# Kernel optimization log

Measured on AMD Instinct MI355X. Metric: run time of the kernel, lower is better.

Reference implementation:

```python
import jax, jax.numpy as jnp
import numpy as np

N = 50000      # nodes
E = 800000     # edges (before self loops)
F_IN = 128     # dataset.num_features
HID = 32       # hidden_channels (per GAT head)
HEADS = 4
C = 40         # dataset.num_classes
NEG_SLOPE = 0.2


def setup_inputs() -> dict:
    key = jax.random.key(0)
    ks = jax.random.split(key, 18)
    g = lambda k, shape, fan: jax.random.normal(k, shape, dtype=jnp.float32) / np.sqrt(fan)
    inp = {
        "x": jax.random.normal(ks[0], (N, F_IN), dtype=jnp.float32),
        "edge_index": jax.random.randint(ks[1], (2, E), 0, N, dtype=jnp.int64),
        # GAT layer 1: F_IN -> HEADS*HID
        "gat_W1": g(ks[2], (F_IN, HEADS * HID), F_IN),
        "gat_att_src1": g(ks[3], (HEADS, HID), HID),
        "gat_att_dst1": g(ks[4], (HEADS, HID), HID),
        "gat_b1": jnp.zeros((HEADS * HID,), jnp.float32),
        # GAT layer 2: HEADS*HID -> C, heads=1
        "gat_W2": g(ks[5], (HEADS * HID, C), HEADS * HID),
        "gat_att_src2": g(ks[6], (1, C), C),
        "gat_att_dst2": g(ks[7], (1, C), C),
        "gat_b2": jnp.zeros((C,), jnp.float32),
        # GCN layers
        "gcn_W1": g(ks[8], (F_IN, HID), F_IN),
        "gcn_b1": jnp.zeros((HID,), jnp.float32),
        "gcn_W2": g(ks[9], (HID, C), HID),
        "gcn_b2": jnp.zeros((C,), jnp.float32),
        # final linear: 2C -> C
        "lin_W": g(ks[10], (2 * C, C), 2 * C),
        "lin_b": jnp.zeros((C,), jnp.float32),
        "weight_c": jnp.float32(0.5),
        "weight_t": jnp.float32(0.5),
    }
    return inp


def _add_self_loops(src, dst, n):
    loop = jnp.arange(n, dtype=src.dtype)
    return jnp.concatenate([src, loop]), jnp.concatenate([dst, loop])


def _gat_conv(x, src, dst, n, W, att_src, att_dst, b, heads, out_dim):
    # h: [n, heads, out_dim]
    h = (x @ W).reshape(n, heads, out_dim)
    a_s = jnp.einsum('nhd,hd->nh', h, att_src)   # source-side attention logit
    a_d = jnp.einsum('nhd,hd->nh', h, att_dst)   # target-side attention logit
    e = jax.nn.leaky_relu(a_s[src] + a_d[dst], NEG_SLOPE)  # [E', heads]
    # softmax over incoming edges of each target node (self loops guarantee >=1 edge)
    m = jax.ops.segment_max(e, dst, num_segments=n)
    ex = jnp.exp(e - m[dst])
    s = jax.ops.segment_sum(ex, dst, num_segments=n)
    alpha = ex / s[dst]                          # [E', heads]
    out = jax.ops.segment_sum(h[src] * alpha[..., None], dst, num_segments=n)
    return out.reshape(n, heads * out_dim) + b


def _gcn_conv(x, src, dst, n, W, b):
    h = x @ W
    deg = jax.ops.segment_sum(jnp.ones(src.shape, h.dtype), dst, num_segments=n)
    norm = jax.lax.rsqrt(deg)                    # deg >= 1 (self loops)
    coef = (norm[src] * norm[dst])[:, None]
    return jax.ops.segment_sum(h[src] * coef, dst, num_segments=n) + b


def reference(x, edge_index, gat_W1, gat_att_src1, gat_att_dst1, gat_b1,
              gat_W2, gat_att_src2, gat_att_dst2, gat_b2,
              gcn_W1, gcn_b1, gcn_W2, gcn_b2, lin_W, lin_b,
              weight_c, weight_t):
    n = x.shape[0]
    src, dst = _add_self_loops(edge_index[0], edge_index[1], n)
    # GAT branch (dropout is identity at inference)
    x_gat = _gat_conv(x, src, dst, n, gat_W1, gat_att_src1, gat_att_dst1,
                      gat_b1, HEADS, HID)
    x_gat = jax.nn.elu(x_gat)
    x_gat = _gat_conv(x_gat, src, dst, n, gat_W2, gat_att_src2, gat_att_dst2,
                      gat_b2, 1, C)
    # GCN branch
    x_gcn = jax.nn.relu(_gcn_conv(x, src, dst, n, gcn_W1, gcn_b1))
    x_gcn = _gcn_conv(x_gcn, src, dst, n, gcn_W2, gcn_b2)
    # weighted feature concat + linear head
    cat = jnp.concatenate([x_gcn * weight_c, x_gat * weight_t], axis=1)  # [n, 2C]
    return cat @ lin_W + lin_b
```

## Files before the change

### kernel.cpp

```cpp
#include <hip/hip_runtime.h>
#include <math.h>

#define F_IN   128
#define HIDC   32
#define NHEAD  4
#define CDIM   40
#define NEG_SLOPE 0.2f
#define BCAP   4096
#define OVCAP  16384
#define SCHUNK 4096

__device__ __forceinline__ float leakyf(float x) { return x > 0.f ? x : NEG_SLOPE * x; }

__device__ __forceinline__ float wred_max(float v) {
#pragma unroll
    for (int o = 32; o > 0; o >>= 1) v = fmaxf(v, __shfl_xor(v, o, 64));
    return v;
}
__device__ __forceinline__ float wred_sum(float v) {
#pragma unroll
    for (int o = 32; o > 0; o >>= 1) v += __shfl_xor(v, o, 64);
    return v;
}
__device__ __forceinline__ float sel4(float4 v, int h) {
    return (h == 0) ? v.x : (h == 1) ? v.y : (h == 2) ? v.z : v.w;
}
__device__ __forceinline__ unsigned pack2_bf16(float a, float b) {
    unsigned ua = __float_as_uint(a);
    unsigned ub = __float_as_uint(b);
    ua = (ua + 0x7FFFu + ((ua >> 16) & 1u)) >> 16;
    ub = (ub + 0x7FFFu + ((ub >> 16) & 1u)) >> 16;
    return ua | (ub << 16);
}
__device__ __forceinline__ float2 unpack2_bf16(unsigned p) {
    return make_float2(__uint_as_float(p << 16), __uint_as_float(p & 0xFFFF0000u));
}

__global__ __launch_bounds__(640) void gemm1_fused_kernel(
    const float* __restrict__ X, const float* __restrict__ Wg,
    const float* __restrict__ Wc, unsigned* __restrict__ h1b,
    unsigned* __restrict__ g1b, int n)
{
    constexpr int BN = 64, BK = 32, CG = 40, NT = 640;
    __shared__ float Xs[BK][BN + 4];
    __shared__ float Ws[BK][160];
    const int tid = threadIdx.x;
    const int cg = tid % CG, ng = tid / CG;
    const int node0 = blockIdx.x * BN;
    float acc[4][4] = {};

    for (int kb = 0; kb < 128; kb += BK) {
        for (int idx = tid; idx < BN * (BK / 4); idx += NT) {
            int nd = idx / (BK / 4);
            int kq = idx % (BK / 4);
            int gnode = node0 + nd;
            float4 v = (gnode < n) ? *(const float4*)&X[(size_t)gnode * 128 + kb + kq * 4]
                                   : make_float4(0.f, 0.f, 0.f, 0.f);
            Xs[kq * 4 + 0][nd] = v.x;
            Xs[kq * 4 + 1][nd] = v.y;
            Xs[kq * 4 + 2][nd] = v.z;
            Xs[kq * 4 + 3][nd] = v.w;
        }
        for (int idx = tid; idx < BK * CG; idx += NT) {
            int kk = idx / CG;
            int cq = idx % CG;
            float4 v = (cq < 32) ? *(const float4*)&Wg[(size_t)(kb + kk) * 128 + cq * 4]
                                 : *(const float4*)&Wc[(size_t)(kb + kk) * 32 + (cq - 32) * 4];
            *(float4*)&Ws[kk][cq * 4] = v;
        }
        __syncthreads();
#pragma unroll
        for (int k = 0; k < BK; ++k) {
            float4 xv = *(const float4*)&Xs[k][ng * 4];
            float4 wv = *(const float4*)&Ws[k][cg * 4];
            float xa[4] = {xv.x, xv.y, xv.z, xv.w};
            float wa[4] = {wv.x, wv.y, wv.z, wv.w};
#pragma unroll
            for (int j = 0; j < 4; ++j)
#pragma unroll
                for (int c = 0; c < 4; ++c)
                    acc[j][c] = fmaf(xa[j], wa[c], acc[j][c]);
        }
        __syncthreads();
    }
#pragma unroll
    for (int j = 0; j < 4; ++j) {
        int gnode = node0 + ng * 4 + j;
        if (gnode >= n) continue;
        uint2 pb = make_uint2(pack2_bf16(acc[j][0], acc[j][1]),
                              pack2_bf16(acc[j][2], acc[j][3]));
        if (cg < 32) *(uint2*)&h1b[(size_t)gnode * 64 + cg * 2] = pb;
        else         *(uint2*)&g1b[(size_t)gnode * 16 + (cg - 32) * 2] = pb;
    }
}

template<int K, int OUTC, int BN, int BK, int OSTRIDE = OUTC>
__global__ __launch_bounds__((OUTC / 4) * (BN / 4)) void gemm_tile(
    const float* __restrict__ X, const float* __restrict__ W,
    const float* __restrict__ bias, float* __restrict__ Y, int n)
{
    constexpr int CG = OUTC / 4;
    constexpr int NG = BN / 4;
    constexpr int NT = CG * NG;
    __shared__ float Xs[BK][BN + 4];
    __shared__ float Ws[BK][OUTC];
    const int tid = threadIdx.x;
    const int cg = tid % CG, ng = tid / CG;
    const int node0 = blockIdx.x * BN;
    float acc[4][4] = {};

    for (int kb = 0; kb < K; kb += BK) {
        for (int idx = tid; idx < BN * (BK / 4); idx += NT) {
            int nd = idx / (BK / 4);
            int kq = idx % (BK / 4);
            int gnode = node0 + nd;
            float4 v = (gnode < n) ? *(const float4*)&X[(size_t)gnode * K + kb + kq * 4]
                                   : make_float4(0.f, 0.f, 0.f, 0.f);
            Xs[kq * 4 + 0][nd] = v.x;
            Xs[kq * 4 + 1][nd] = v.y;
            Xs[kq * 4 + 2][nd] = v.z;
            Xs[kq * 4 + 3][nd] = v.w;
        }
        for (int idx = tid; idx < BK * CG; idx += NT) {
            int kk = idx / CG;
            int cq = idx % CG;
            *(float4*)&Ws[kk][cq * 4] = *(const float4*)&W[(size_t)(kb + kk) * OUTC + cq * 4];
        }
        __syncthreads();
#pragma unroll
        for (int k = 0; k < BK; ++k) {
            float4 xv = *(const float4*)&Xs[k][ng * 4];
            float4 wv = *(const float4*)&Ws[k][cg * 4];
            float xa[4] = {xv.x, xv.y, xv.z, xv.w};
            float wa[4] = {wv.x, wv.y, wv.z, wv.w};
#pragma unroll
            for (int j = 0; j < 4; ++j)
#pragma unroll
                for (int c = 0; c < 4; ++c)
                    acc[j][c] = fmaf(xa[j], wa[c], acc[j][c]);
        }
        __syncthreads();
    }

    float4 bv = make_float4(0.f, 0.f, 0.f, 0.f);
    if (bias) bv = *(const float4*)&bias[cg * 4];
#pragma unroll
    for (int j = 0; j < 4; ++j) {
        int gnode = node0 + ng * 4 + j;
        if (gnode < n) {
            float4 o = make_float4(acc[j][0] + bv.x, acc[j][1] + bv.y,
                                   acc[j][2] + bv.z, acc[j][3] + bv.w);
            *(float4*)&Y[(size_t)gnode * OSTRIDE + cg * 4] = o;
        }
    }
}

template<int K, int OUTC, int BN, int BK, int OSTRIDE_U, int OFF_U>
__global__ __launch_bounds__((OUTC / 4) * (BN / 4)) void gemm_tile_b(
    const float* __restrict__ X, const float* __restrict__ W,
    unsigned* __restrict__ Yb, int n)
{
    constexpr int CG = OUTC / 4;
    constexpr int NG = BN / 4;
    constexpr int NT = CG * NG;
    __shared__ float Xs[BK][BN + 4];
    __shared__ float Ws[BK][OUTC];
    const int tid = threadIdx.x;
    const int cg = tid % CG, ng = tid / CG;
    const int node0 = blockIdx.x * BN;
    float acc[4][4] = {};

    for (int kb = 0; kb < K; kb += BK) {
        for (int idx = tid; idx < BN * (BK / 4); idx += NT) {
            int nd = idx / (BK / 4);
            int kq = idx % (BK / 4);
            int gnode = node0 + nd;
            float4 v = (gnode < n) ? *(const float4*)&X[(size_t)gnode * K + kb + kq * 4]
                                   : make_float4(0.f, 0.f, 0.f, 0.f);
            Xs[kq * 4 + 0][nd] = v.x;
            Xs[kq * 4 + 1][nd] = v.y;
            Xs[kq * 4 + 2][nd] = v.z;
            Xs[kq * 4 + 3][nd] = v.w;
        }
        for (int idx = tid; idx < BK * CG; idx += NT) {
            int kk = idx / CG;
            int cq = idx % CG;
            *(float4*)&Ws[kk][cq * 4] = *(const float4*)&W[(size_t)(kb + kk) * OUTC + cq * 4];
        }
        __syncthreads();
#pragma unroll
        for (int k = 0; k < BK; ++k) {
            float4 xv = *(const float4*)&Xs[k][ng * 4];
            float4 wv = *(const float4*)&Ws[k][cg * 4];
            float xa[4] = {xv.x, xv.y, xv.z, xv.w};
            float wa[4] = {wv.x, wv.y, wv.z, wv.w};
#pragma unroll
            for (int j = 0; j < 4; ++j)
#pragma unroll
                for (int c = 0; c < 4; ++c)
                    acc[j][c] = fmaf(xa[j], wa[c], acc[j][c]);
        }
        __syncthreads();
    }

#pragma unroll
    for (int j = 0; j < 4; ++j) {
        int gnode = node0 + ng * 4 + j;
        if (gnode < n) {
            uint2 pb = make_uint2(pack2_bf16(acc[j][0], acc[j][1]),
                                  pack2_bf16(acc[j][2], acc[j][3]));
            *(uint2*)&Yb[(size_t)gnode * OSTRIDE_U + OFF_U + cg * 2] = pb;
        }
    }
}

template<int K, int OUTC, int BN, int BK, int OSTRIDE_U, int OFF_U>
__global__ __launch_bounds__((OUTC / 4) * (BN / 4)) void gemm_tile_bb(
    const unsigned* __restrict__ Xb, const float* __restrict__ W,
    unsigned* __restrict__ Yb, int n)
{
    constexpr int CG = OUTC / 4;
    constexpr int NG = BN / 4;
    constexpr int NT = CG * NG;
    __shared__ float Xs[BK][BN + 4];
    __shared__ float Ws[BK][OUTC];
    const int tid = threadIdx.x;
    const int cg = tid % CG, ng = tid / CG;
    const int node0 = blockIdx.x * BN;
    float acc[4][4] = {};

    for (int kb = 0; kb < K; kb += BK) {
        for (int idx = tid; idx < BN * (BK / 8); idx += NT) {
            int nd = idx / (BK / 8);
            int kq = idx % (BK / 8);
            int gnode = node0 + nd;
            uint4 v = (gnode < n) ? *(const uint4*)&Xb[(size_t)gnode * (K / 2) + kb / 2 + kq * 4]
                                  : make_uint4(0u, 0u, 0u, 0u);
            float2 a = unpack2_bf16(v.x), b = unpack2_bf16(v.y);
            float2 c = unpack2_bf16(v.z), d = unpack2_bf16(v.w);
            Xs[kq * 8 + 0][nd] = a.x; Xs[kq * 8 + 1][nd] = a.y;
            Xs[kq * 8 + 2][nd] = b.x; Xs[kq * 8 + 3][nd] = b.y;
            Xs[kq * 8 + 4][nd] = c.x; Xs[kq * 8 + 5][nd] = c.y;
            Xs[kq * 8 + 6][nd] = d.x; Xs[kq * 8 + 7][nd] = d.y;
        }
        for (int idx = tid; idx < BK * CG; idx += NT) {
            int kk = idx / CG;
            int cq = idx % CG;
            *(float4*)&Ws[kk][cq * 4] = *(const float4*)&W[(size_t)(kb + kk) * OUTC + cq * 4];
        }
        __syncthreads();
#pragma unroll
        for (int k = 0; k < BK; ++k) {
            float4 xv = *(const float4*)&Xs[k][ng * 4];
            float4 wv = *(const float4*)&Ws[k][cg * 4];
            float xa[4] = {xv.x, xv.y, xv.z, xv.w};
            float wa[4] = {wv.x, wv.y, wv.z, wv.w};
#pragma unroll
            for (int j = 0; j < 4; ++j)
#pragma unroll
                for (int c = 0; c < 4; ++c)
                    acc[j][c] = fmaf(xa[j], wa[c], acc[j][c]);
        }
        __syncthreads();
    }

#pragma unroll
    for (int j = 0; j < 4; ++j) {
        int gnode = node0 + ng * 4 + j;
        if (gnode < n) {
            uint2 pb = make_uint2(pack2_bf16(acc[j][0], acc[j][1]),
                                  pack2_bf16(acc[j][2], acc[j][3]));
            *(uint2*)&Yb[(size_t)gnode * OSTRIDE_U + OFF_U + cg * 2] = pb;
        }
    }
}

__global__ __launch_bounds__(256) void bucket_scatter_kernel(
    const int* __restrict__ src, const int* __restrict__ dst,
    unsigned* __restrict__ bcnt, unsigned* __restrict__ bpair,
    unsigned* __restrict__ ovf_cnt, uint2* __restrict__ ovf, int e, int nbuck)
{
    __shared__ unsigned hist[512];
    __shared__ unsigned base[512];
    const int t = threadIdx.x;
    const int lo = blockIdx.x * SCHUNK;
    const int hi = min(lo + SCHUNK, e);
    for (int i = t; i < nbuck; i += 256) hist[i] = 0;
    __syncthreads();
    for (int i = lo + t; i < hi; i += 256)
        atomicAdd(&hist[((unsigned)dst[i]) >> 7], 1u);
    __syncthreads();
    for (int i = t; i < nbuck; i += 256) {
        unsigned c = hist[i];
        base[i] = c ? atomicAdd(&bcnt[i], c) : 0u;
        hist[i] = 0;
    }
    __syncthreads();
    for (int i = lo + t; i < hi; i += 256) {
        unsigned s = (unsigned)src[i], d = (unsigned)dst[i];
        unsigned b = d >> 7;
        unsigned pos = base[b] + atomicAdd(&hist[b], 1u);
        if (pos < BCAP) bpair[(size_t)b * BCAP + pos] = s | ((d & 127u) << 16);
        else {
            unsigned o = atomicAdd(ovf_cnt, 1u);
            if (o < OVCAP) ovf[o] = make_uint2(s, d);
        }
    }
}

__global__ __launch_bounds__(256) void bucket_count_kernel(
    const unsigned* __restrict__ bcnt, const unsigned* __restrict__ bpair,
    const unsigned* __restrict__ ovf_cnt, const uint2* __restrict__ ovf,
    unsigned* __restrict__ counts, int n)
{
    __shared__ unsigned lc[128];
    const int b = blockIdx.x, base = b << 7;
    if (threadIdx.x < 128) lc[threadIdx.x] = 0;
    __syncthreads();
    unsigned bc = bcnt[b];
    int cnt = (int)(bc < BCAP ? bc : BCAP);
    for (int k = threadIdx.x; k < cnt; k += 256)
        atomicAdd(&lc[bpair[(size_t)b * BCAP + k] >> 16], 1u);
    unsigned oc_u = *ovf_cnt;
    int oc = (int)(oc_u < OVCAP ? oc_u : OVCAP);
    for (int k = threadIdx.x; k < oc; k += 256) {
        uint2 pp = ovf[k];
        if ((int)(pp.y >> 7) == b) atomicAdd(&lc[pp.y & 127u], 1u);
    }
    __syncthreads();
    int i = base + threadIdx.x;
    if (threadIdx.x < 128 && i < n) counts[i] = lc[threadIdx.x];
}

__global__ __launch_bounds__(256) void scan_reduce_kernel(const unsigned* __restrict__ counts,
                                                          unsigned* __restrict__ partials, int n)
{
    __shared__ unsigned sm[256];
    int t = threadIdx.x;
    int i = blockIdx.x * 256 + t;
    unsigned v = (i < n) ? counts[i] : 0u;
    sm[t] = v;
    __syncthreads();
#pragma unroll
    for (int off = 128; off > 0; off >>= 1) {
        if (t < off) sm[t] += sm[t + off];
        __syncthreads();
    }
    if (t == 0) partials[blockIdx.x] = sm[0];
}

__global__ __launch_bounds__(256) void scan_partials_kernel(unsigned* __restrict__ partials,
                                                            unsigned* __restrict__ rs, int nb, int n)
{
    __shared__ unsigned sm[256];
    int t = threadIdx.x;
    unsigned v = (t < nb) ? partials[t] : 0u;
    sm[t] = v;
    __syncthreads();
#pragma unroll
    for (int off = 1; off < 256; off <<= 1) {
        unsigned u = (t >= off) ? sm[t - off] : 0u;
        __syncthreads();
        sm[t] += u;
        __syncthreads();
    }
    if (t < nb) partials[t] = sm[t] - v;
    if (t == 255) rs[n] = sm[255];
}

__global__ __launch_bounds__(256) void scan_write_kernel(const unsigned* __restrict__ counts,
                                                         const unsigned* __restrict__ partials,
                                                         unsigned* __restrict__ rs,
                                                         float* __restrict__ nrm, int n)
{
    __shared__ unsigned sm[256];
    int t = threadIdx.x;
    int i = blockIdx.x * 256 + t;
    unsigned c = (i < n) ? counts[i] : 0u;
    sm[t] = c;
    __syncthreads();
#pragma unroll
    for (int off = 1; off < 256; off <<= 1) {
        unsigned u = (t >= off) ? sm[t - off] : 0u;
        __syncthreads();
        sm[t] += u;
        __syncthreads();
    }
    if (i < n) {
        rs[i] = partials[blockIdx.x] + sm[t] - c;
        nrm[i] = rsqrtf((float)(c + 1u));
    }
}

__global__ __launch_bounds__(256) void bucket_place_kernel(
    const unsigned* __restrict__ bcnt, const unsigned* __restrict__ bpair,
    const unsigned* __restrict__ rs, unsigned* __restrict__ csr_src,
    unsigned* __restrict__ cursor, int n)
{
    __shared__ unsigned lc[128];
    __shared__ unsigned rbase[128];
    const int b = blockIdx.x, base = b << 7;
    if (threadIdx.x < 128) {
        lc[threadIdx.x] = 0;
        int i = base + threadIdx.x;
        rbase[threadIdx.x] = (i < n) ? rs[i] : 0u;
    }
    __syncthreads();
    unsigned bc = bcnt[b];
    int cnt = (int)(bc < BCAP ? bc : BCAP);
    for (int k = threadIdx.x; k < cnt; k += 256) {
        unsigned v = bpair[(size_t)b * BCAP + k];
        unsigned ld = v >> 16;
        unsigned r = atomicAdd(&lc[ld], 1u);
        csr_src[rbase[ld] + r] = v & 0xFFFFu;
    }
    __syncthreads();
    int i = base + threadIdx.x;
    if (threadIdx.x < 128 && i < n) cursor[i] = rbase[threadIdx.x] + lc[threadIdx.x];
}

__global__ void overflow_fill_kernel(const unsigned* __restrict__ ovf_cnt,
                                     const uint2* __restrict__ ovf,
                                     unsigned* __restrict__ cursor,
                                     unsigned* __restrict__ csr_src)
{
    unsigned oc_u = *ovf_cnt;
    int oc = (int)(oc_u < OVCAP ? oc_u : OVCAP);
    for (int k = threadIdx.x; k < oc; k += 256) {
        uint2 pp = ovf[k];
        unsigned pos = atomicAdd(&cursor[pp.y], 1u);
        csr_src[pos] = pp.x;
    }
}

__global__ void logits1_kernel(const unsigned* __restrict__ h1b, const float* __restrict__ aw_s,
                               const float* __restrict__ aw_d, float* __restrict__ as1,
                               float* __restrict__ ad1, int n)
{
    __shared__ float sw[128], dw[128];
    if (threadIdx.x < 128) { sw[threadIdx.x] = aw_s[threadIdx.x]; dw[threadIdx.x] = aw_d[threadIdx.x]; }
    __syncthreads();
    int idx = blockIdx.x * 256 + threadIdx.x;
    if (idx >= n * NHEAD) return;
    int node = idx >> 2, h = idx & 3;
    const unsigned* row = h1b + (size_t)node * 64 + h * 16;
    float s = 0.f, d = 0.f;
#pragma unroll
    for (int k = 0; k < 16; ++k) {
        float2 v = unpack2_bf16(row[k]);
        int c = h * HIDC + 2 * k;
        s = fmaf(v.x, sw[c], s);     s = fmaf(v.y, sw[c + 1], s);
        d = fmaf(v.x, dw[c], d);     d = fmaf(v.y, dw[c + 1], d);
    }
    as1[idx] = s; ad1[idx] = d;
}

__global__ void logits2_kernel(const unsigned* __restrict__ hg_b, const float* __restrict__ aw_s,
                               const float* __restrict__ aw_d, float* __restrict__ as2,
                               float* __restrict__ ad2, int n)
{
    __shared__ float sw[CDIM], dw[CDIM];
    if (threadIdx.x < CDIM) { sw[threadIdx.x] = aw_s[threadIdx.x]; dw[threadIdx.x] = aw_d[threadIdx.x]; }
    __syncthreads();
    int i = blockIdx.x * 256 + threadIdx.x;
    if (i >= n) return;
    const unsigned* row = hg_b + (size_t)i * 40;
    float s = 0.f, d = 0.f;
#pragma unroll
    for (int k = 0; k < 20; ++k) {
        float2 v = unpack2_bf16(row[k]);
        s = fmaf(v.x, sw[2 * k], s);     s = fmaf(v.y, sw[2 * k + 1], s);
        d = fmaf(v.x, dw[2 * k], d);     d = fmaf(v.y, dw[2 * k + 1], d);
    }
    as2[i] = s; ad2[i] = d;
}

#define CAP1 96
__global__ __launch_bounds__(256) void gat_agg1_kernel(
    const unsigned* __restrict__ h1b,
    const float* __restrict__ as1, const float* __restrict__ ad1,
    const unsigned* __restrict__ rs, const unsigned* __restrict__ csr_src,
    const float* __restrict__ b1, unsigned* __restrict__ xgb, int n)
{
    __shared__ unsigned sidx[4][CAP1];
    __shared__ float    w4[4][CAP1][4];
    const int wid = threadIdx.x >> 6;
    const int lane = threadIdx.x & 63;
    const int i = blockIdx.x * 4 + wid;
    if (i >= n) return;
    const unsigned beg = rs[i];
    const int deg = (int)(rs[i + 1] - beg);
    const float4* as1v = (const float4*)as1;
    float4 av = as1v[i];
    float4 dv = ((const float4*)ad1)[i];
    float4 es = make_float4(leakyf(av.x + dv.x), leakyf(av.y + dv.y),
                            leakyf(av.z + dv.z), leakyf(av.w + dv.w));
    float m0 = es.x, m1 = es.y, m2 = es.z, m3 = es.w;
    for (int k = lane; k < deg; k += 64) {
        unsigned s = csr_src[beg + k];
        float4 a = as1v[s];
        float e0 = leakyf(a.x + dv.x), e1 = leakyf(a.y + dv.y);
        float e2 = leakyf(a.z + dv.z), e3 = leakyf(a.w + dv.w);
        if (k < CAP1) {
            sidx[wid][k] = s;
            w4[wid][k][0] = e0; w4[wid][k][1] = e1;
            w4[wid][k][2] = e2; w4[wid][k][3] = e3;
        }
        m0 = fmaxf(m0, e0); m1 = fmaxf(m1, e1);
        m2 = fmaxf(m2, e2); m3 = fmaxf(m3, e3);
    }
    m0 = wred_max(m0); m1 = wred_max(m1); m2 = wred_max(m2); m3 = wred_max(m3);
    float s0 = 0.f, s1 = 0.f, s2 = 0.f, s3 = 0.f;
    if (lane == 0) {
        s0 = __expf(es.x - m0); s1 = __expf(es.y - m1);
        s2 = __expf(es.z - m2); s3 = __expf(es.w - m3);
    }
    const int dc = deg < CAP1 ? deg : CAP1;
    for (int k = lane; k < dc; k += 64) {
        float w0 = __expf(w4[wid][k][0] - m0); w4[wid][k][0] = w0; s0 += w0;
        float w1 = __expf(w4[wid][k][1] - m1); w4[wid][k][1] = w1; s1 += w1;
        float w2 = __expf(w4[wid][k][2] - m2); w4[wid][k][2] = w2; s2 += w2;
        float w3 = __expf(w4[wid][k][3] - m3); w4[wid][k][3] = w3; s3 += w3;
    }
    for (int k = CAP1 + lane; k < deg; k += 64) {
        unsigned s = csr_src[beg + k];
        float4 a = as1v[s];
        s0 += __expf(leakyf(a.x + dv.x) - m0);
        s1 += __expf(leakyf(a.y + dv.y) - m1);
        s2 += __expf(leakyf(a.z + dv.z) - m2);
        s3 += __expf(leakyf(a.w + dv.w) - m3);
    }
    s0 = wred_sum(s0); s1 = wred_sum(s1); s2 = wred_sum(s2); s3 = wred_sum(s3);
    __threadfence_block();
    const int h = lane >> 4;
    const float mh   = sel4(make_float4(m0, m1, m2, m3), h);
    const float advh = sel4(dv, h);
    const float ssh  = sel4(make_float4(s0, s1, s2, s3), h);
    const float wself = __expf(sel4(es, h) - mh);
    float2 hv = unpack2_bf16(h1b[(size_t)i * 64 + lane]);
    float2 acc = make_float2(hv.x * wself, hv.y * wself);
    auto edge = [&](int j, unsigned& s, float& w) {
        if (j < CAP1) { s = sidx[wid][j]; w = w4[wid][j][h]; }
        else {
            s = csr_src[beg + j];
            float4 a = as1v[s];
            w = __expf(leakyf(sel4(a, h) + advh) - mh);
        }
    };
    int j = 0;
    for (; j + 4 <= deg; j += 4) {
        unsigned sa, sb, sc, sd; float wa, wb, wc, wd;
        edge(j, sa, wa); edge(j + 1, sb, wb); edge(j + 2, sc, wc); edge(j + 3, sd, wd);
        float2 va = unpack2_bf16(h1b[(size_t)sa * 64 + lane]);
        float2 vb = unpack2_bf16(h1b[(size_t)sb * 64 + lane]);
        float2 vc = unpack2_bf16(h1b[(size_t)sc * 64 + lane]);
        float2 vd = unpack2_bf16(h1b[(size_t)sd * 64 + lane]);
        acc.x = fmaf(va.x, wa, acc.x); acc.y = fmaf(va.y, wa, acc.y);
        acc.x = fmaf(vb.x, wb, acc.x); acc.y = fmaf(vb.y, wb, acc.y);
        acc.x = fmaf(vc.x, wc, acc.x); acc.y = fmaf(vc.y, wc, acc.y);
        acc.x = fmaf(vd.x, wd, acc.x); acc.y = fmaf(vd.y, wd, acc.y);
    }
    for (; j < deg; ++j) {
        unsigned s; float w; edge(j, s, w);
        float2 v = unpack2_bf16(h1b[(size_t)s * 64 + lane]);
        acc.x = fmaf(v.x, w, acc.x); acc.y = fmaf(v.y, w, acc.y);
    }
    float inv = 1.f / ssh;
    int c0 = 2 * lane;
    float o0 = acc.x * inv + b1[c0];
    float o1 = acc.y * inv + b1[c0 + 1];
    o0 = o0 > 0.f ? o0 : __expf(o0) - 1.f;
    o1 = o1 > 0.f ? o1 : __expf(o1) - 1.f;
    xgb[(size_t)i * 64 + lane] = pack2_bf16(o0, o1);
}

#define CAP2 128
__global__ __launch_bounds__(256) void agg2_fused_kernel(
    const unsigned* __restrict__ hg_b, const float* __restrict__ as2,
    const float* __restrict__ ad2, const float* __restrict__ nrm,
    const unsigned* __restrict__ rs, const unsigned* __restrict__ csr_src,
    const float* __restrict__ gat_b2, const float* __restrict__ gcn_b2,
    const float* __restrict__ wc_p, const float* __restrict__ wt_p,
    float* __restrict__ cat, int n)
{
    __shared__ unsigned sidx[4][CAP2];
    __shared__ float    wgt[4][CAP2];
    __shared__ float    cf [4][CAP2];
    const int wid = threadIdx.x >> 6;
    const int lane = threadIdx.x & 63;
    const int i = blockIdx.x * 4 + wid;
    if (i >= n) return;
    const unsigned beg = rs[i];
    const int deg = (int)(rs[i + 1] - beg);
    const float adv = ad2[i];
    const float e_self = leakyf(as2[i] + adv);
    const float ni = nrm[i];
    float m = e_self;
    for (int k = lane; k < deg; k += 64) {
        unsigned s = csr_src[beg + k];
        float e = leakyf(as2[s] + adv);
        if (k < CAP2) { sidx[wid][k] = s; wgt[wid][k] = e; cf[wid][k] = nrm[s]; }
        m = fmaxf(m, e);
    }
    m = wred_max(m);
    float ssum = (lane == 0) ? __expf(e_self - m) : 0.f;
    const int dc = deg < CAP2 ? deg : CAP2;
    for (int k = lane; k < dc; k += 64) {
        float w = __expf(wgt[wid][k] - m);
        wgt[wid][k] = w; ssum += w;
    }
    for (int k = CAP2 + lane; k < deg; k += 64) {
        unsigned s = csr_src[beg + k];
        ssum += __expf(leakyf(as2[s] + adv) - m);
    }
    ssum = wred_sum(ssum);
    __threadfence_block();
    const bool act   = lane < 40;
    const bool isgat = lane < 20;
    const float selfw = isgat ? __expf(e_self - m) : ni * ni;
    float2 acc = make_float2(0.f, 0.f);
    if (act) {
        float2 v = unpack2_bf16(hg_b[(size_t)i * 40 + lane]);
        acc.x = v.x * selfw; acc.y = v.y * selfw;
    }
    auto edge = [&](int j, unsigned& s, float& w) {
        if (j < CAP2) {
            s = sidx[wid][j];
            w = isgat ? wgt[wid][j] : cf[wid][j] * ni;
        } else {
            s = csr_src[beg + j];
            w = isgat ? __expf(leakyf(as2[s] + adv) - m) : nrm[s] * ni;
        }
    };
    int j = 0;
    for (; j + 4 <= deg; j += 4) {
        unsigned sa, sb, sc, sd; float wa, wb, wc, wd;
        edge(j, sa, wa); edge(j + 1, sb, wb); edge(j + 2, sc, wc); edge(j + 3, sd, wd);
        if (act) {
            float2 va = unpack2_bf16(hg_b[(size_t)sa * 40 + lane]);
            float2 vb = unpack2_bf16(hg_b[(size_t)sb * 40 + lane]);
            float2 vc = unpack2_bf16(hg_b[(size_t)sc * 40 + lane]);
            float2 vd = unpack2_bf16(hg_b[(size_t)sd * 40 + lane]);
            acc.x = fmaf(va.x, wa, acc.x); acc.y = fmaf(va.y, wa, acc.y);
            acc.x = fmaf(vb.x, wb, acc.x); acc.y = fmaf(vb.y, wb, acc.y);
            acc.x = fmaf(vc.x, wc, acc.x); acc.y = fmaf(vc.y, wc, acc.y);
            acc.x = fmaf(vd.x, wd, acc.x); acc.y = fmaf(vd.y, wd, acc.y);
        }
    }
    for (; j < deg; ++j) {
        unsigned s; float w; edge(j, s, w);
        if (act) {
            float2 v = unpack2_bf16(hg_b[(size_t)s * 40 + lane]);
            acc.x = fmaf(v.x, w, acc.x); acc.y = fmaf(v.y, w, acc.y);
        }
    }
    if (act) {
        if (isgat) {
            float inv = 1.f / ssum, wt = *wt_p;
            int c0 = 2 * lane;
            cat[(size_t)i * 80 + 40 + c0]     = (acc.x * inv + gat_b2[c0]) * wt;
            cat[(size_t)i * 80 + 40 + c0 + 1] = (acc.y * inv + gat_b2[c0 + 1]) * wt;
        } else {
            float wc = *wc_p;
            int c0 = 2 * (lane - 20);
            cat[(size_t)i * 80 + c0]     = (acc.x + gcn_b2[c0]) * wc;
            cat[(size_t)i * 80 + c0 + 1] = (acc.y + gcn_b2[c0 + 1]) * wc;
        }
    }
}

#define CAPG 128
__global__ __launch_bounds__(256) void gcn_agg1_kernel(
    const unsigned short* __restrict__ g1b, const float* __restrict__ nrm,
    const unsigned* __restrict__ rs, const unsigned* __restrict__ csr_src,
    const float* __restrict__ b, float* __restrict__ out, int n)
{
    __shared__ unsigned sidx[4][CAPG];
    __shared__ float    cf[4][CAPG];
    const int wid = threadIdx.x >> 6;
    const int lane = threadIdx.x & 63;
    const int i = blockIdx.x * 4 + wid;
    if (i >= n) return;
    const unsigned beg = rs[i];
    const int deg = (int)(rs[i + 1] - beg);
    const float ni = nrm[i];
    const int dcg = deg < CAPG ? deg : CAPG;
    for (int k = lane; k < dcg; k += 64) {
        unsigned s = csr_src[beg + k];
        sidx[wid][k] = s; cf[wid][k] = nrm[s];
    }
    __threadfence_block();
    const int half = lane >> 5, c = lane & 31;
    auto ldb = [&](unsigned node) {
        return __uint_as_float(((unsigned)g1b[(size_t)node * 32 + c]) << 16);
    };
    float acc = (half == 0) ? ldb(i) * ni * ni : 0.f;
    auto edge = [&](int j, unsigned& s, float& w) {
        if (j < CAPG) { s = sidx[wid][j]; w = cf[wid][j] * ni; }
        else { s = csr_src[beg + j]; w = nrm[s] * ni; }
    };
    int j = half;
    for (; j + 2 < deg; j += 4) {
        unsigned sa, sb; float wa, wb;
        edge(j, sa, wa); edge(j + 2, sb, wb);
        float va = ldb(sa);
        float vb = ldb(sb);
        acc = fmaf(va, wa, acc);
        acc = fmaf(vb, wb, acc);
    }
    for (; j < deg; j += 2) {
        unsigned s; float w; edge(j, s, w);
        acc = fmaf(ldb(s), w, acc);
    }
    acc += __shfl_xor(acc, 32, 64);
    if (half == 0) out[(size_t)i * 32 + c] = fmaxf(acc + b[c], 0.f);
}

extern "C" void kernel_launch(void* const* d_in, const int* in_sizes, int n_in,
                              void* d_out, int out_size, void* d_ws, size_t ws_size,
                              hipStream_t stream)
{
    const float* x        = (const float*)d_in[0];
    const int*   eidx     = (const int*)d_in[1];
    const float* gat_W1   = (const float*)d_in[2];
    const float* att_s1   = (const float*)d_in[3];
    const float* att_d1   = (const float*)d_in[4];
    const float* gat_b1   = (const float*)d_in[5];
    const float* gat_W2   = (const float*)d_in[6];
    const float* att_s2   = (const float*)d_in[7];
    const float* att_d2   = (const float*)d_in[8];
    const float* gat_b2   = (const float*)d_in[9];
    const float* gcn_W1   = (const float*)d_in[10];
    const float* gcn_b1   = (const float*)d_in[11];
    const float* gcn_W2   = (const float*)d_in[12];
    const float* gcn_b2   = (const float*)d_in[13];
    const float* lin_W    = (const float*)d_in[14];
    const float* lin_b    = (const float*)d_in[15];
    const float* wc_p     = (const float*)d_in[16];
    const float* wt_p     = (const float*)d_in[17];

    const int n = in_sizes[0] / F_IN;
    const int e = in_sizes[1] / 2;
    const int* src = eidx;
    const int* dst = eidx + e;
    const int NBUCK = (n + 127) >> 7;

    char* p = (char*)d_ws;
    auto alloc = [&](size_t bytes) -> void* {
        void* r = (void*)p;
        p += (bytes + 255) & ~(size_t)255;
        return r;
    };
    unsigned* counts  = (unsigned*)alloc((size_t)n * 4);
    unsigned* rs      = (unsigned*)alloc((size_t)(n + 1) * 4);
    unsigned* cursor  = (unsigned*)alloc((size_t)n * 4);
    unsigned* partials= (unsigned*)alloc(256 * 4);
    unsigned* bcnt    = (unsigned*)alloc((size_t)(NBUCK + 1) * 4);
    unsigned* csr_src = (unsigned*)alloc((size_t)e * 4);
    float* nrm     = (float*)alloc((size_t)n * 4);
    float* as1     = (float*)alloc((size_t)n * 4 * 4);
    float* ad1     = (float*)alloc((size_t)n * 4 * 4);
    float* as2     = (float*)alloc((size_t)n * 4);
    float* ad2     = (float*)alloc((size_t)n * 4);
    float* cat     = (float*)alloc((size_t)n * 80 * 4);
    unsigned* hg_b = (unsigned*)alloc((size_t)n * 40 * 4);
    float* xg      = (float*)alloc((size_t)n * F_IN * 4);
    unsigned* g1b  = (unsigned*)alloc((size_t)n * 16 * 4);
    unsigned* bpair = (unsigned*)cat;
    uint2*    ovf   = (uint2*)(bpair + (size_t)NBUCK * BCAP);
    unsigned* h1b   = (unsigned*)cat;
    float*    gacc1 = xg;
    unsigned* xgb   = (unsigned*)xg;
    unsigned* ovf_cnt = bcnt + NBUCK;

    const int NB = (n + 255) / 256;
    const int WB = (n + 3) / 4;
    const int SB = (e + SCHUNK - 1) / SCHUNK;

    hipMemsetAsync(bcnt, 0, (size_t)(NBUCK + 1) * 4, stream);
    bucket_scatter_kernel<<<SB, 256, 0, stream>>>(src, dst, bcnt, bpair, ovf_cnt, ovf, e, NBUCK);
    bucket_count_kernel<<<NBUCK, 256, 0, stream>>>(bcnt, bpair, ovf_cnt, ovf, counts, n);
    scan_reduce_kernel<<<NB, 256, 0, stream>>>(counts, partials, n);
    scan_partials_kernel<<<1, 256, 0, stream>>>(partials, rs, NB, n);
    scan_write_kernel<<<NB, 256, 0, stream>>>(counts, partials, rs, nrm, n);
    bucket_place_kernel<<<NBUCK, 256, 0, stream>>>(bcnt, bpair, rs, csr_src, cursor, n);
    overflow_fill_kernel<<<1, 256, 0, stream>>>(ovf_cnt, ovf, cursor, csr_src);

    gemm1_fused_kernel<<<(n + 63) / 64, 640, 0, stream>>>(x, gat_W1, gcn_W1, h1b, g1b, n);

    gcn_agg1_kernel<<<WB, 256, 0, stream>>>((const unsigned short*)g1b, nrm, rs, csr_src,
                                            gcn_b1, gacc1, n);
    gemm_tile_b<32, 40, 128, 32, 40, 20><<<(n + 127) / 128, 320, 0, stream>>>(gacc1, gcn_W2, hg_b, n);

    logits1_kernel<<<(n * 4 + 255) / 256, 256, 0, stream>>>(h1b, att_s1, att_d1, as1, ad1, n);
    gat_agg1_kernel<<<WB, 256, 0, stream>>>(h1b, as1, ad1, rs, csr_src, gat_b1, xgb, n);
    gemm_tile_bb<128, 40, 128, 32, 40, 0><<<(n + 127) / 128, 320, 0, stream>>>(xgb, gat_W2, hg_b, n);
    logits2_kernel<<<NB, 256, 0, stream>>>(hg_b, att_s2, att_d2, as2, ad2, n);

    agg2_fused_kernel<<<WB, 256, 0, stream>>>(hg_b, as2, ad2, nrm, rs, csr_src,
                                              gat_b2, gcn_b2, wc_p, wt_p, cat, n);

    gemm_tile<80, 40, 128, 40><<<(n + 127) / 128, 320, 0, stream>>>(cat, lin_W, lin_b, (float*)d_out, n);
}
```

Baseline: 360.1 us.

## Use bf16 MFMA for first fused GEMM and fold layer-1 attention logits into it

Replaces the FP32 FMA tiled GEMM that computes the fused GAT/GCN first-layer projection with a bf16 MFMA (16x16x32) kernel, adding a small prep kernel that packs the weights into the MFMA B-fragment layout. The accumulated tile is staged in shared memory, and the per-head source/destination attention logits are computed there, which removes the separate logits1 kernel and its re-read of h1b. X is now rounded to bf16 before multiplication, so precision drops slightly compared to the FP32 accumulate path. An extra tiny kernel launch is added for the weight packing.

```diff
diff --git a/kernel.cpp b/kernel.cpp
--- a/kernel.cpp
+++ b/kernel.cpp
@@ -10,6 +10,9 @@
 #define OVCAP  16384
 #define SCHUNK 4096
 
+typedef __attribute__((ext_vector_type(8))) short bf16x8;
+typedef __attribute__((ext_vector_type(4))) float f32x4;
+
 __device__ __forceinline__ float leakyf(float x) { return x > 0.f ? x : NEG_SLOPE * x; }
 
 __device__ __forceinline__ float wred_max(float v) {
@@ -36,61 +39,96 @@
     return make_float2(__uint_as_float(p << 16), __uint_as_float(p & 0xFFFF0000u));
 }
 
-__global__ __launch_bounds__(640) void gemm1_fused_kernel(
-    const float* __restrict__ X, const float* __restrict__ Wg,
-    const float* __restrict__ Wc, unsigned* __restrict__ h1b,
-    unsigned* __restrict__ g1b, int n)
-{
-    constexpr int BN = 64, BK = 32, CG = 40, NT = 640;
-    __shared__ float Xs[BK][BN + 4];
-    __shared__ float Ws[BK][160];
+__global__ void wb_prep_kernel(const float* __restrict__ Wg, const float* __restrict__ Wc,
+                               uint4* __restrict__ wbf)
+{
+    int b = blockIdx.x;
+    int lane = threadIdx.x;
+    int nt = b >> 2, ks = b & 3;
+    int c = nt * 16 + (lane & 15);
+    int k0 = ks * 32 + (lane >> 4) * 8;
+    unsigned u[4];
+#pragma unroll
+    for (int jj = 0; jj < 4; ++jj) {
+        int k = k0 + 2 * jj;
+        float a0 = (c < 128) ? Wg[(size_t)k * 128 + c] : Wc[(size_t)k * 32 + (c - 128)];
+        float a1 = (c < 128) ? Wg[(size_t)(k + 1) * 128 + c] : Wc[(size_t)(k + 1) * 32 + (c - 128)];
+        u[jj] = pack2_bf16(a0, a1);
+    }
+    wbf[(size_t)b * 64 + lane] = make_uint4(u[0], u[1], u[2], u[3]);
+}
+
+__global__ __launch_bounds__(256) void gemm1_mfma_kernel(
+    const float* __restrict__ X, const uint4* __restrict__ wbf,
+    const float* __restrict__ aw_s, const float* __restrict__ aw_d,
+    unsigned* __restrict__ h1b, unsigned* __restrict__ g1b,
+    float* __restrict__ as1, float* __restrict__ ad1, int n)
+{
+    __shared__ float Ct[64][164];
+    __shared__ float sw[128], dw[128];
     const int tid = threadIdx.x;
-    const int cg = tid % CG, ng = tid / CG;
-    const int node0 = blockIdx.x * BN;
-    float acc[4][4] = {};
-
-    for (int kb = 0; kb < 128; kb += BK) {
-        for (int idx = tid; idx < BN * (BK / 4); idx += NT) {
-            int nd = idx / (BK / 4);
-            int kq = idx % (BK / 4);
-            int gnode = node0 + nd;
-            float4 v = (gnode < n) ? *(const float4*)&X[(size_t)gnode * 128 + kb + kq * 4]
-                                   : make_float4(0.f, 0.f, 0.f, 0.f);
-            Xs[kq * 4 + 0][nd] = v.x;
-            Xs[kq * 4 + 1][nd] = v.y;
-            Xs[kq * 4 + 2][nd] = v.z;
-            Xs[kq * 4 + 3][nd] = v.w;
-        }
-        for (int idx = tid; idx < BK * CG; idx += NT) {
-            int kk = idx / CG;
-            int cq = idx % CG;
-            float4 v = (cq < 32) ? *(const float4*)&Wg[(size_t)(kb + kk) * 128 + cq * 4]
-                                 : *(const float4*)&Wc[(size_t)(kb + kk) * 32 + (cq - 32) * 4];
-            *(float4*)&Ws[kk][cq * 4] = v;
-        }
-        __syncthreads();
-#pragma unroll
-        for (int k = 0; k < BK; ++k) {
-            float4 xv = *(const float4*)&Xs[k][ng * 4];
-            float4 wv = *(const float4*)&Ws[k][cg * 4];
-            float xa[4] = {xv.x, xv.y, xv.z, xv.w};
-            float wa[4] = {wv.x, wv.y, wv.z, wv.w};
-#pragma unroll
-            for (int j = 0; j < 4; ++j)
-#pragma unroll
-                for (int c = 0; c < 4; ++c)
-                    acc[j][c] = fmaf(xa[j], wa[c], acc[j][c]);
-        }
-        __syncthreads();
-    }
-#pragma unroll
-    for (int j = 0; j < 4; ++j) {
-        int gnode = node0 + ng * 4 + j;
-        if (gnode >= n) continue;
-        uint2 pb = make_uint2(pack2_bf16(acc[j][0], acc[j][1]),
-                              pack2_bf16(acc[j][2], acc[j][3]));
-        if (cg < 32) *(uint2*)&h1b[(size_t)gnode * 64 + cg * 2] = pb;
-        else         *(uint2*)&g1b[(size_t)gnode * 16 + (cg - 32) * 2] = pb;
+    const int w = tid >> 6, lane = tid & 63;
+    const int m = lane & 15, q = lane >> 4;
+    const int node0 = blockIdx.x * 64;
+    if (tid < 128) { sw[tid] = aw_s[tid]; dw[tid] = aw_d[tid]; }
+
+    f32x4 acc[10];
+#pragma unroll
+    for (int t = 0; t < 10; ++t) acc[t] = (f32x4){0.f, 0.f, 0.f, 0.f};
+
+    const int row = node0 + w * 16 + m;
+    const bool rv = row < n;
+#pragma unroll
+    for (int ks = 0; ks < 4; ++ks) {
+        uint4 pa = make_uint4(0u, 0u, 0u, 0u);
+        if (rv) {
+            const float* xr = X + (size_t)row * 128 + ks * 32 + q * 8;
+            float4 a0 = *(const float4*)xr;
+            float4 a1 = *(const float4*)(xr + 4);
+            pa = make_uint4(pack2_bf16(a0.x, a0.y), pack2_bf16(a0.z, a0.w),
+                            pack2_bf16(a1.x, a1.y), pack2_bf16(a1.z, a1.w));
+        }
+        bf16x8 af = *(bf16x8*)&pa;
+#pragma unroll
+        for (int nt = 0; nt < 10; ++nt) {
+            uint4 pb = wbf[(size_t)(nt * 4 + ks) * 64 + lane];
+            bf16x8 bfv = *(bf16x8*)&pb;
+            acc[nt] = __builtin_amdgcn_mfma_f32_16x16x32_bf16(af, bfv, acc[nt], 0, 0, 0);
+        }
+    }
+#pragma unroll
+    for (int nt = 0; nt < 10; ++nt)
+#pragma unroll
+        for (int r = 0; r < 4; ++r)
+            Ct[w * 16 + q * 4 + r][nt * 16 + m] = acc[nt][r];
+    __syncthreads();
+
+    for (int i = tid; i < 64 * 64; i += 256) {
+        int nd = i >> 6, u = i & 63;
+        int gn = node0 + nd;
+        if (gn < n)
+            h1b[(size_t)gn * 64 + u] = pack2_bf16(Ct[nd][2 * u], Ct[nd][2 * u + 1]);
+    }
+    for (int i = tid; i < 64 * 16; i += 256) {
+        int nd = i >> 4, u = i & 15;
+        int gn = node0 + nd;
+        if (gn < n)
+            g1b[(size_t)gn * 16 + u] = pack2_bf16(Ct[nd][128 + 2 * u], Ct[nd][128 + 2 * u + 1]);
+    }
+    {
+        int nd = tid >> 2, h = tid & 3;
+        int gn = node0 + nd;
+        if (gn < n) {
+            float s = 0.f, d = 0.f;
+#pragma unroll
+            for (int k = 0; k < HIDC; ++k) {
+                float v = Ct[nd][h * HIDC + k];
+                s = fmaf(v, sw[h * HIDC + k], s);
+                d = fmaf(v, dw[h * HIDC + k], d);
+            }
+            as1[(size_t)gn * 4 + h] = s;
+            ad1[(size_t)gn * 4 + h] = d;
+        }
     }
 }
 
@@ -431,28 +469,6 @@
         unsigned pos = atomicAdd(&cursor[pp.y], 1u);
         csr_src[pos] = pp.x;
     }
-}
-
-__global__ void logits1_kernel(const unsigned* __restrict__ h1b, const float* __restrict__ aw_s,
-                               const float* __restrict__ aw_d, float* __restrict__ as1,
-                               float* __restrict__ ad1, int n)
-{
-    __shared__ float sw[128], dw[128];
-    if (threadIdx.x < 128) { sw[threadIdx.x] = aw_s[threadIdx.x]; dw[threadIdx.x] = aw_d[threadIdx.x]; }
-    __syncthreads();
-    int idx = blockIdx.x * 256 + threadIdx.x;
-    if (idx >= n * NHEAD) return;
-    int node = idx >> 2, h = idx & 3;
-    const unsigned* row = h1b + (size_t)node * 64 + h * 16;
-    float s = 0.f, d = 0.f;
-#pragma unroll
-    for (int k = 0; k < 16; ++k) {
-        float2 v = unpack2_bf16(row[k]);
-        int c = h * HIDC + 2 * k;
-        s = fmaf(v.x, sw[c], s);     s = fmaf(v.y, sw[c + 1], s);
-        d = fmaf(v.x, dw[c], d);     d = fmaf(v.y, dw[c + 1], d);
-    }
-    as1[idx] = s; ad1[idx] = d;
 }
 
 __global__ void logits2_kernel(const unsigned* __restrict__ hg_b, const float* __restrict__ aw_s,
@@ -757,6 +773,7 @@
     unsigned* partials= (unsigned*)alloc(256 * 4);
     unsigned* bcnt    = (unsigned*)alloc((size_t)(NBUCK + 1) * 4);
     unsigned* csr_src = (unsigned*)alloc((size_t)e * 4);
+    uint4*    wbf     = (uint4*)alloc(40 * 64 * 16);
     float* nrm     = (float*)alloc((size_t)n * 4);
     float* as1     = (float*)alloc((size_t)n * 4 * 4);
     float* ad1     = (float*)alloc((size_t)n * 4 * 4);
@@ -786,13 +803,14 @@
     bucket_place_kernel<<<NBUCK, 256, 0, stream>>>(bcnt, bpair, rs, csr_src, cursor, n);
     overflow_fill_kernel<<<1, 256, 0, stream>>>(ovf_cnt, ovf, cursor, csr_src);
 
-    gemm1_fused_kernel<<<(n + 63) / 64, 640, 0, stream>>>(x, gat_W1, gcn_W1, h1b, g1b, n);
+    wb_prep_kernel<<<40, 64, 0, stream>>>(gat_W1, gcn_W1, wbf);
+    gemm1_mfma_kernel<<<(n + 63) / 64, 256, 0, stream>>>(x, wbf, att_s1, att_d1,
+                                                         h1b, g1b, as1, ad1, n);
 
     gcn_agg1_kernel<<<WB, 256, 0, stream>>>((const unsigned short*)g1b, nrm, rs, csr_src,
                                             gcn_b1, gacc1, n);
     gemm_tile_b<32, 40, 128, 32, 40, 20><<<(n + 127) / 128, 320, 0, stream>>>(gacc1, gcn_W2, hg_b, n);
 
-    logits1_kernel<<<(n * 4 + 255) / 256, 256, 0, stream>>>(h1b, att_s1, att_d1, as1, ad1, n);
     gat_agg1_kernel<<<WB, 256, 0, stream>>>(h1b, as1, ad1, rs, csr_src, gat_b1, xgb, n);
     gemm_tile_bb<128, 40, 128, 32, 40, 0><<<(n + 127) / 128, 320, 0, stream>>>(xgb, gat_W2, hg_b, n);
     logits2_kernel<<<NB, 256, 0, stream>>>(hg_b, att_s2, att_d2, as2, ad2, n);
```

Result: faster. 340.3 us (-5.5%).
